# Optimization experiments

Measured on AMD Instinct MI355X. Metric: run time of the kernel, lower is better.

Reference implementation:

```python
import jax, jax.numpy as jnp
import numpy as np

N_NODES = 50000
N_EDGES = 800000
N_GRAPHS = 64
F_IN, HID, EMB = 6, 64, 128


def gcn_conv(x, edge_index, W, b):
    """PyG GCNConv: add self-loops, symmetric deg^{-1/2} normalization, scatter-add."""
    n = x.shape[0]
    loop = jnp.arange(n)
    src = jnp.concatenate([edge_index[0], loop])
    dst = jnp.concatenate([edge_index[1], loop])
    deg = jnp.zeros((n,), x.dtype).at[dst].add(1.0)
    dinv = jnp.where(deg > 0, jax.lax.rsqrt(deg), 0.0)
    norm = dinv[src] * dinv[dst]              # [E+n]
    h = x @ W                                  # [n, out]
    msg = h[src] * norm[:, None]               # gather + scale
    out = jnp.zeros((n, W.shape[1]), h.dtype).at[dst].add(msg)  # scatter-add
    return out + b


def global_mean_pool(x, batch, num_graphs):
    sums = jax.ops.segment_sum(x, batch, num_segments=num_graphs)
    cnts = jax.ops.segment_sum(jnp.ones((x.shape[0],), x.dtype), batch, num_segments=num_graphs)
    return sums / jnp.maximum(cnts, 1.0)[:, None]


def setup_inputs() -> dict:
    key = jax.random.key(0)
    ks = jax.random.split(key, 12)
    x = jax.random.normal(ks[0], (N_NODES, F_IN), dtype=jnp.float32)
    edge_index = jax.random.randint(ks[1], (2, N_EDGES), 0, N_NODES, dtype=jnp.int64 if jax.config.jax_enable_x64 else jnp.int32)
    batch = jnp.sort(jax.random.randint(ks[2], (N_NODES,), 0, N_GRAPHS, dtype=jnp.int32))
    def glorot(k, shp):
        lim = float(np.sqrt(6.0 / (shp[0] + shp[1])))
        return jax.random.uniform(k, shp, jnp.float32, -lim, lim)
    return {
        "x": x, "edge_index": edge_index, "batch": batch,
        "W1": glorot(ks[3], (F_IN, HID)), "b1": jnp.zeros((HID,), jnp.float32),
        "W2": glorot(ks[4], (HID, HID)),  "b2": jnp.zeros((HID,), jnp.float32),
        "W3": glorot(ks[5], (HID, HID)),  "b3": jnp.zeros((HID,), jnp.float32),
        "Wfc": glorot(ks[6], (HID, EMB)), "bfc": jnp.zeros((EMB,), jnp.float32),
    }


def reference(x, edge_index, batch, W1, b1, W2, b2, W3, b3, Wfc, bfc):
    h = jax.nn.relu(gcn_conv(x, edge_index, W1, b1))
    h = jax.nn.relu(gcn_conv(h, edge_index, W2, b2))
    h = jax.nn.relu(gcn_conv(h, edge_index, W3, b3))
    g = global_mean_pool(h, batch, N_GRAPHS)     # [num_graphs, HID]
    return jax.nn.relu(g @ Wfc + bfc)            # [num_graphs, EMB]
```

## Files before the change

kernel.cpp:

```cpp
#include <hip/hip_runtime.h>

#define N_NODES 50000
#define N_EDGES 800000
#define N_GRAPHS 64
#define F_IN 6
#define HID 64
#define EMB 128

#define NBINS 196
#define EPB 4096
#define NCHUNK ((N_EDGES + EPB - 1) / EPB)
#define EPT (EPB / 256)

__global__ void k_init(int* __restrict__ bin_cnt) {
    if (threadIdx.x < NBINS + 4) bin_cnt[threadIdx.x] = 0;
}

__global__ void k_binhist(const int* __restrict__ dst, int* __restrict__ bin_cnt) {
    __shared__ int lcnt[NBINS];
    for (int b = threadIdx.x; b < NBINS; b += 256) lcnt[b] = 0;
    __syncthreads();
    int e0 = blockIdx.x * EPB;
#pragma unroll
    for (int t = 0; t < EPT; ++t) {
        int e = e0 + t * 256 + threadIdx.x;
        if (e < N_EDGES) atomicAdd(&lcnt[dst[e] >> 8], 1);
    }
    __syncthreads();
    for (int b = threadIdx.x; b < NBINS; b += 256) {
        int c = lcnt[b];
        if (c) atomicAdd(&bin_cnt[b], c);
    }
}

__global__ void k_binscan(const int* __restrict__ bin_cnt, int* __restrict__ bin_start,
                          int* __restrict__ bin_pos, int* __restrict__ row_start,
                          float* __restrict__ gsum, float* __restrict__ gcnt) {
    __shared__ int s[256];
    int t = threadIdx.x;
    int v = (t < NBINS) ? bin_cnt[t] : 0;
    s[t] = v;
    __syncthreads();
    for (int off = 1; off < 256; off <<= 1) {
        int o = (t >= off) ? s[t - off] : 0;
        __syncthreads();
        s[t] += o;
        __syncthreads();
    }
    if (t < NBINS) { int st = s[t] - v; bin_start[t] = st; bin_pos[t] = st; }
    if (t == 0) { bin_start[NBINS] = N_EDGES; row_start[N_NODES] = N_EDGES; }
    for (int i = t; i < N_GRAPHS * HID; i += 256) gsum[i] = 0.0f;
    if (t < N_GRAPHS) gcnt[t] = 0.0f;
}

__global__ void k_part(const int* __restrict__ src, const int* __restrict__ dst,
                       int* __restrict__ bin_pos, int* __restrict__ rec) {
    __shared__ int lcnt[NBINS];
    __shared__ int lbase[NBINS];
    for (int b = threadIdx.x; b < NBINS; b += 256) lcnt[b] = 0;
    __syncthreads();
    int e0 = blockIdx.x * EPB;
    int myBin[EPT], myRank[EPT], myRec[EPT];
#pragma unroll
    for (int t = 0; t < EPT; ++t) {
        int e = e0 + t * 256 + threadIdx.x;
        myBin[t] = -1;
        if (e < N_EDGES) {
            int d = dst[e];
            int s = src[e];
            int b = d >> 8;
            myBin[t] = b;
            myRec[t] = (s << 8) | (d & 255);
            myRank[t] = atomicAdd(&lcnt[b], 1);
        }
    }
    __syncthreads();
    for (int b = threadIdx.x; b < NBINS; b += 256) {
        int c = lcnt[b];
        lbase[b] = c ? atomicAdd(&bin_pos[b], c) : 0;
    }
    __syncthreads();
#pragma unroll
    for (int t = 0; t < EPT; ++t)
        if (myBin[t] >= 0) rec[lbase[myBin[t]] + myRank[t]] = myRec[t];
}

__global__ void k_bindeg(const int* __restrict__ rec, const int* __restrict__ bin_start,
                         const float* __restrict__ x, int* __restrict__ row_start,
                         float* __restrict__ dinv, float* __restrict__ xs) {
    __shared__ int ldeg[256];
    __shared__ int s[256];
    int t = threadIdx.x;
    ldeg[t] = 0;
    __syncthreads();
    int beg = bin_start[blockIdx.x], end = bin_start[blockIdx.x + 1];
    for (int r = beg + t; r < end; r += 256)
        atomicAdd(&ldeg[rec[r] & 255], 1);
    __syncthreads();
    int v = ldeg[t];
    s[t] = v;
    __syncthreads();
    for (int off = 1; off < 256; off <<= 1) {
        int o = (t >= off) ? s[t - off] : 0;
        __syncthreads();
        s[t] += o;
        __syncthreads();
    }
    int node = blockIdx.x * 256 + t;
    if (node < N_NODES) {
        row_start[node] = beg + s[t] - v;
        float dv = rsqrtf((float)(v + 1));
        dinv[node] = dv;
#pragma unroll
        for (int k = 0; k < F_IN; ++k) xs[node * F_IN + k] = x[node * F_IN + k] * dv;
    }
}

__global__ void k_fine(const int* __restrict__ rec, const int* __restrict__ bin_start,
                       const int* __restrict__ row_start, int* __restrict__ eidx) {
    __shared__ int lpos[256];
    lpos[threadIdx.x] = 0;
    __syncthreads();
    int beg = bin_start[blockIdx.x], end = bin_start[blockIdx.x + 1];
    int base = blockIdx.x * 256;
    for (int r = beg + threadIdx.x; r < end; r += 256) {
        int rc = rec[r];
        int ld = rc & 255;
        int p = atomicAdd(&lpos[ld], 1);
        eidx[row_start[base + ld] + p] = rc >> 8;
    }
}

__device__ __forceinline__ float bcast(float v, int lane) {
    return __int_as_float(__builtin_amdgcn_readlane(__float_as_int(v), lane));
}

__global__ void k_l1(const float* __restrict__ xs, const int* __restrict__ row_start,
                     const int* __restrict__ eidx, const float* __restrict__ dinv,
                     const float* __restrict__ W1, const float* __restrict__ b1,
                     float* __restrict__ out) {
    __shared__ float sW[F_IN * HID];
    __shared__ float sB[HID];
    for (int i = threadIdx.x; i < F_IN * HID; i += 256) sW[i] = W1[i];
    if (threadIdx.x < HID) sB[threadIdx.x] = b1[threadIdx.x];
    __syncthreads();
    int node = (blockIdx.x * blockDim.x + threadIdx.x) >> 6;
    int f = threadIdx.x & 63;
    if (node >= N_NODES) return;
    int beg = __builtin_amdgcn_readfirstlane(row_start[node]);
    int end = __builtin_amdgcn_readfirstlane(row_start[node + 1]);
    bool act = (f < F_IN);
    float sum = 0.0f;
    int j = beg;
    for (; j + 8 <= end; j += 8) {
        int s0 = eidx[j+0], s1 = eidx[j+1], s2 = eidx[j+2], s3 = eidx[j+3];
        int s4 = eidx[j+4], s5 = eidx[j+5], s6 = eidx[j+6], s7 = eidx[j+7];
        if (act) {
            float v0 = xs[s0 * F_IN + f], v1 = xs[s1 * F_IN + f];
            float v2 = xs[s2 * F_IN + f], v3 = xs[s3 * F_IN + f];
            float v4 = xs[s4 * F_IN + f], v5 = xs[s5 * F_IN + f];
            float v6 = xs[s6 * F_IN + f], v7 = xs[s7 * F_IN + f];
            sum += ((v0 + v1) + (v2 + v3)) + ((v4 + v5) + (v6 + v7));
        }
    }
    for (; j < end; ++j) {
        int s = eidx[j];
        if (act) sum += xs[s * F_IN + f];
    }
    float dv = dinv[node];
    float val = act ? (sum + xs[node * F_IN + f]) * dv : 0.0f;
    float o = sB[f];
    o = fmaf(bcast(val, 0), sW[0 * HID + f], o);
    o = fmaf(bcast(val, 1), sW[1 * HID + f], o);
    o = fmaf(bcast(val, 2), sW[2 * HID + f], o);
    o = fmaf(bcast(val, 3), sW[3 * HID + f], o);
    o = fmaf(bcast(val, 4), sW[4 * HID + f], o);
    o = fmaf(bcast(val, 5), sW[5 * HID + f], o);
    out[node * HID + f] = fmaxf(o, 0.0f);
}

#define MM_BLOCKS 625
__global__ void k_mm(const float* __restrict__ x, const float* __restrict__ W,
                     const float* __restrict__ dinv, float* __restrict__ h) {
    int f = threadIdx.x & 63;
    float wk[HID];
#pragma unroll
    for (int k = 0; k < HID; ++k) wk[k] = W[k * HID + f];
    int wv = blockIdx.x * (blockDim.x >> 6) + (threadIdx.x >> 6);
    const int nwaves = MM_BLOCKS * 4;
    for (int node = wv; node < N_NODES; node += nwaves) {
        float xv = x[node * HID + f];
        float dv = dinv[node];
        float a0 = 0.0f, a1 = 0.0f, a2 = 0.0f, a3 = 0.0f;
#pragma unroll
        for (int k = 0; k < HID; k += 4) {
            a0 = fmaf(bcast(xv, k + 0), wk[k + 0], a0);
            a1 = fmaf(bcast(xv, k + 1), wk[k + 1], a1);
            a2 = fmaf(bcast(xv, k + 2), wk[k + 2], a2);
            a3 = fmaf(bcast(xv, k + 3), wk[k + 3], a3);
        }
        h[node * HID + f] = ((a0 + a1) + (a2 + a3)) * dv;
    }
}

__global__ void k_gather(const float* __restrict__ h, const int* __restrict__ row_start,
                         const int* __restrict__ eidx, const float* __restrict__ dinv,
                         const float* __restrict__ b, float* __restrict__ out) {
    int node = (blockIdx.x * blockDim.x + threadIdx.x) >> 6;
    int f = threadIdx.x & 63;
    if (node >= N_NODES) return;
    int beg = __builtin_amdgcn_readfirstlane(row_start[node]);
    int end = __builtin_amdgcn_readfirstlane(row_start[node + 1]);
    float sum = 0.0f;
    int j = beg;
    for (; j + 8 <= end; j += 8) {
        int s0 = eidx[j+0], s1 = eidx[j+1], s2 = eidx[j+2], s3 = eidx[j+3];
        int s4 = eidx[j+4], s5 = eidx[j+5], s6 = eidx[j+6], s7 = eidx[j+7];
        float v0 = h[s0 * HID + f], v1 = h[s1 * HID + f];
        float v2 = h[s2 * HID + f], v3 = h[s3 * HID + f];
        float v4 = h[s4 * HID + f], v5 = h[s5 * HID + f];
        float v6 = h[s6 * HID + f], v7 = h[s7 * HID + f];
        sum += ((v0 + v1) + (v2 + v3)) + ((v4 + v5) + (v6 + v7));
    }
    if (j + 4 <= end) {
        int s0 = eidx[j+0], s1 = eidx[j+1], s2 = eidx[j+2], s3 = eidx[j+3];
        float v0 = h[s0 * HID + f], v1 = h[s1 * HID + f];
        float v2 = h[s2 * HID + f], v3 = h[s3 * HID + f];
        sum += ((v0 + v1) + (v2 + v3));
        j += 4;
    }
    for (; j < end; ++j) sum += h[eidx[j] * HID + f];
    sum += h[node * HID + f];
    out[node * HID + f] = fmaxf(fmaf(sum, dinv[node], b[f]), 0.0f);
}

#define POOL_BLOCKS 200
__global__ void k_pool(const float* __restrict__ x, const int* __restrict__ batch,
                       float* __restrict__ gsum, float* __restrict__ gcnt) {
    const int npb = (N_NODES + POOL_BLOCKS - 1) / POOL_BLOCKS;
    int start = blockIdx.x * npb;
    int end = start + npb;
    if (end > N_NODES) end = N_NODES;
    int f = threadIdx.x & 63;
    int grp = threadIdx.x >> 6;
    float sum = 0.0f, cnt = 0.0f;
    int curg = -1;
    for (int node = start + grp; node < end; node += 4) {
        int g = batch[node];
        if (g != curg) {
            if (curg >= 0) {
                atomicAdd(&gsum[curg * HID + f], sum);
                if (f == 0) atomicAdd(&gcnt[curg], cnt);
            }
            curg = g; sum = 0.0f; cnt = 0.0f;
        }
        sum += x[node * HID + f];
        cnt += 1.0f;
    }
    if (curg >= 0) {
        atomicAdd(&gsum[curg * HID + f], sum);
        if (f == 0) atomicAdd(&gcnt[curg], cnt);
    }
}

__global__ void k_fc(const float* __restrict__ gsum, const float* __restrict__ gcnt,
                     const float* __restrict__ Wfc, const float* __restrict__ bfc,
                     float* __restrict__ out) {
    int gid = blockIdx.x * blockDim.x + threadIdx.x;
    if (gid >= N_GRAPHS * EMB) return;
    int g = gid >> 7;
    int j = gid & 127;
    float inv = 1.0f / fmaxf(gcnt[g], 1.0f);
    float s = bfc[j];
#pragma unroll 8
    for (int k = 0; k < HID; ++k) s += gsum[g * HID + k] * inv * Wfc[k * EMB + j];
    out[gid] = fmaxf(s, 0.0f);
}

extern "C" void kernel_launch(void* const* d_in, const int* in_sizes, int n_in,
                              void* d_out, int out_size, void* d_ws, size_t ws_size,
                              hipStream_t stream) {
    const float* x    = (const float*)d_in[0];
    const int*   ei   = (const int*)d_in[1];
    const int*   batch= (const int*)d_in[2];
    const float* W1   = (const float*)d_in[3];
    const float* b1   = (const float*)d_in[4];
    const float* W2   = (const float*)d_in[5];
    const float* b2   = (const float*)d_in[6];
    const float* W3   = (const float*)d_in[7];
    const float* b3   = (const float*)d_in[8];
    const float* Wfc  = (const float*)d_in[9];
    const float* bfc  = (const float*)d_in[10];
    float* out = (float*)d_out;

    float* ws        = (float*)d_ws;
    float* dinv      = ws;
    float* h         = ws + 50048;
    float* xcur      = h + N_NODES * HID;
    float* gsum      = xcur + N_NODES * HID;
    float* gcnt      = gsum + N_GRAPHS * HID;
    float* xs        = gcnt + 64;
    int*   row_start = (int*)(xs + 300032);
    int*   bin_cnt   = row_start + 50176;
    int*   bin_start = bin_cnt + 256;
    int*   bin_pos   = bin_start + 256;
    int*   rec       = bin_pos + 256;
    int*   eidx      = rec + 800000;

    const int* src = ei;
    const int* dst = ei + N_EDGES;

    const int B = 256;
    const int gNF = (N_NODES * HID + B - 1) / B;

    k_init<<<1, B, 0, stream>>>(bin_cnt);
    k_binhist<<<NCHUNK, B, 0, stream>>>(dst, bin_cnt);
    k_binscan<<<1, B, 0, stream>>>(bin_cnt, bin_start, bin_pos, row_start, gsum, gcnt);
    k_part<<<NCHUNK, B, 0, stream>>>(src, dst, bin_pos, rec);
    k_bindeg<<<NBINS, B, 0, stream>>>(rec, bin_start, x, row_start, dinv, xs);
    k_fine<<<NBINS, B, 0, stream>>>(rec, bin_start, row_start, eidx);

    k_l1<<<gNF, B, 0, stream>>>(xs, row_start, eidx, dinv, W1, b1, xcur);
    k_mm<<<MM_BLOCKS, B, 0, stream>>>(xcur, W2, dinv, h);
    k_gather<<<gNF, B, 0, stream>>>(h, row_start, eidx, dinv, b2, xcur);
    k_mm<<<MM_BLOCKS, B, 0, stream>>>(xcur, W3, dinv, h);
    k_gather<<<gNF, B, 0, stream>>>(h, row_start, eidx, dinv, b3, xcur);

    k_pool<<<POOL_BLOCKS, B, 0, stream>>>(xcur, batch, gsum, gcnt);
    k_fc<<<(N_GRAPHS * EMB + B - 1) / B, B, 0, stream>>>(gsum, gcnt, Wfc, bfc, out);
}
```

Measured before the change: 206.7 us.

## Fuse neighbor aggregation with following dense transform into persistent kernels

Merges layer-1 aggregation with the W2 matmul, and layer-2 gather with the W3 matmul, into two persistent wave-per-node kernels. The intermediate activations no longer round-trip through global memory, and two launches are removed. In exchange, each wave holds 64 weight registers while gathering, which may lower occupancy and latency hiding in the gather loop, and grid-stride scheduling over 1280 blocks replaces the one-node-per-wave grid.

```diff
diff --git a/kernel.cpp b/kernel.cpp
--- a/kernel.cpp
+++ b/kernel.cpp
@@ -135,71 +135,109 @@
     return __int_as_float(__builtin_amdgcn_readlane(__float_as_int(v), lane));
 }
 
-__global__ void k_l1(const float* __restrict__ xs, const int* __restrict__ row_start,
-                     const int* __restrict__ eidx, const float* __restrict__ dinv,
-                     const float* __restrict__ W1, const float* __restrict__ b1,
-                     float* __restrict__ out) {
+#define PB 1280
+
+__global__ void k_l1mm(const float* __restrict__ xs, const int* __restrict__ row_start,
+                       const int* __restrict__ eidx, const float* __restrict__ dinv,
+                       const float* __restrict__ W1, const float* __restrict__ b1,
+                       const float* __restrict__ W2, float* __restrict__ hout) {
     __shared__ float sW[F_IN * HID];
     __shared__ float sB[HID];
     for (int i = threadIdx.x; i < F_IN * HID; i += 256) sW[i] = W1[i];
     if (threadIdx.x < HID) sB[threadIdx.x] = b1[threadIdx.x];
     __syncthreads();
-    int node = (blockIdx.x * blockDim.x + threadIdx.x) >> 6;
-    int f = threadIdx.x & 63;
-    if (node >= N_NODES) return;
-    int beg = __builtin_amdgcn_readfirstlane(row_start[node]);
-    int end = __builtin_amdgcn_readfirstlane(row_start[node + 1]);
-    bool act = (f < F_IN);
-    float sum = 0.0f;
-    int j = beg;
-    for (; j + 8 <= end; j += 8) {
-        int s0 = eidx[j+0], s1 = eidx[j+1], s2 = eidx[j+2], s3 = eidx[j+3];
-        int s4 = eidx[j+4], s5 = eidx[j+5], s6 = eidx[j+6], s7 = eidx[j+7];
-        if (act) {
-            float v0 = xs[s0 * F_IN + f], v1 = xs[s1 * F_IN + f];
-            float v2 = xs[s2 * F_IN + f], v3 = xs[s3 * F_IN + f];
-            float v4 = xs[s4 * F_IN + f], v5 = xs[s5 * F_IN + f];
-            float v6 = xs[s6 * F_IN + f], v7 = xs[s7 * F_IN + f];
-            sum += ((v0 + v1) + (v2 + v3)) + ((v4 + v5) + (v6 + v7));
-        }
-    }
-    for (; j < end; ++j) {
-        int s = eidx[j];
-        if (act) sum += xs[s * F_IN + f];
-    }
-    float dv = dinv[node];
-    float val = act ? (sum + xs[node * F_IN + f]) * dv : 0.0f;
-    float o = sB[f];
-    o = fmaf(bcast(val, 0), sW[0 * HID + f], o);
-    o = fmaf(bcast(val, 1), sW[1 * HID + f], o);
-    o = fmaf(bcast(val, 2), sW[2 * HID + f], o);
-    o = fmaf(bcast(val, 3), sW[3 * HID + f], o);
-    o = fmaf(bcast(val, 4), sW[4 * HID + f], o);
-    o = fmaf(bcast(val, 5), sW[5 * HID + f], o);
-    out[node * HID + f] = fmaxf(o, 0.0f);
-}
-
-#define MM_BLOCKS 625
-__global__ void k_mm(const float* __restrict__ x, const float* __restrict__ W,
-                     const float* __restrict__ dinv, float* __restrict__ h) {
     int f = threadIdx.x & 63;
     float wk[HID];
 #pragma unroll
-    for (int k = 0; k < HID; ++k) wk[k] = W[k * HID + f];
-    int wv = blockIdx.x * (blockDim.x >> 6) + (threadIdx.x >> 6);
-    const int nwaves = MM_BLOCKS * 4;
-    for (int node = wv; node < N_NODES; node += nwaves) {
-        float xv = x[node * HID + f];
+    for (int k = 0; k < HID; ++k) wk[k] = W2[k * HID + f];
+    bool act = (f < F_IN);
+    int wv = blockIdx.x * 4 + (threadIdx.x >> 6);
+    for (int node = wv; node < N_NODES; node += PB * 4) {
+        int beg = __builtin_amdgcn_readfirstlane(row_start[node]);
+        int end = __builtin_amdgcn_readfirstlane(row_start[node + 1]);
+        float sum = 0.0f;
+        int j = beg;
+        for (; j + 8 <= end; j += 8) {
+            int s0 = eidx[j+0], s1 = eidx[j+1], s2 = eidx[j+2], s3 = eidx[j+3];
+            int s4 = eidx[j+4], s5 = eidx[j+5], s6 = eidx[j+6], s7 = eidx[j+7];
+            if (act) {
+                float v0 = xs[s0 * F_IN + f], v1 = xs[s1 * F_IN + f];
+                float v2 = xs[s2 * F_IN + f], v3 = xs[s3 * F_IN + f];
+                float v4 = xs[s4 * F_IN + f], v5 = xs[s5 * F_IN + f];
+                float v6 = xs[s6 * F_IN + f], v7 = xs[s7 * F_IN + f];
+                sum += ((v0 + v1) + (v2 + v3)) + ((v4 + v5) + (v6 + v7));
+            }
+        }
+        for (; j < end; ++j) {
+            int s = eidx[j];
+            if (act) sum += xs[s * F_IN + f];
+        }
         float dv = dinv[node];
+        float val = act ? (sum + xs[node * F_IN + f]) * dv : 0.0f;
+        float o = sB[f];
+        o = fmaf(bcast(val, 0), sW[0 * HID + f], o);
+        o = fmaf(bcast(val, 1), sW[1 * HID + f], o);
+        o = fmaf(bcast(val, 2), sW[2 * HID + f], o);
+        o = fmaf(bcast(val, 3), sW[3 * HID + f], o);
+        o = fmaf(bcast(val, 4), sW[4 * HID + f], o);
+        o = fmaf(bcast(val, 5), sW[5 * HID + f], o);
+        o = fmaxf(o, 0.0f);
         float a0 = 0.0f, a1 = 0.0f, a2 = 0.0f, a3 = 0.0f;
 #pragma unroll
         for (int k = 0; k < HID; k += 4) {
-            a0 = fmaf(bcast(xv, k + 0), wk[k + 0], a0);
-            a1 = fmaf(bcast(xv, k + 1), wk[k + 1], a1);
-            a2 = fmaf(bcast(xv, k + 2), wk[k + 2], a2);
-            a3 = fmaf(bcast(xv, k + 3), wk[k + 3], a3);
-        }
-        h[node * HID + f] = ((a0 + a1) + (a2 + a3)) * dv;
+            a0 = fmaf(bcast(o, k + 0), wk[k + 0], a0);
+            a1 = fmaf(bcast(o, k + 1), wk[k + 1], a1);
+            a2 = fmaf(bcast(o, k + 2), wk[k + 2], a2);
+            a3 = fmaf(bcast(o, k + 3), wk[k + 3], a3);
+        }
+        hout[node * HID + f] = ((a0 + a1) + (a2 + a3)) * dv;
+    }
+}
+
+__global__ void k_gmm(const float* __restrict__ h, const int* __restrict__ row_start,
+                      const int* __restrict__ eidx, const float* __restrict__ dinv,
+                      const float* __restrict__ b2, const float* __restrict__ W3,
+                      float* __restrict__ hout) {
+    int f = threadIdx.x & 63;
+    float wk[HID];
+#pragma unroll
+    for (int k = 0; k < HID; ++k) wk[k] = W3[k * HID + f];
+    float bv = b2[f];
+    int wv = blockIdx.x * 4 + (threadIdx.x >> 6);
+    for (int node = wv; node < N_NODES; node += PB * 4) {
+        int beg = __builtin_amdgcn_readfirstlane(row_start[node]);
+        int end = __builtin_amdgcn_readfirstlane(row_start[node + 1]);
+        float sum = 0.0f;
+        int j = beg;
+        for (; j + 8 <= end; j += 8) {
+            int s0 = eidx[j+0], s1 = eidx[j+1], s2 = eidx[j+2], s3 = eidx[j+3];
+            int s4 = eidx[j+4], s5 = eidx[j+5], s6 = eidx[j+6], s7 = eidx[j+7];
+            float v0 = h[s0 * HID + f], v1 = h[s1 * HID + f];
+            float v2 = h[s2 * HID + f], v3 = h[s3 * HID + f];
+            float v4 = h[s4 * HID + f], v5 = h[s5 * HID + f];
+            float v6 = h[s6 * HID + f], v7 = h[s7 * HID + f];
+            sum += ((v0 + v1) + (v2 + v3)) + ((v4 + v5) + (v6 + v7));
+        }
+        if (j + 4 <= end) {
+            int s0 = eidx[j+0], s1 = eidx[j+1], s2 = eidx[j+2], s3 = eidx[j+3];
+            float v0 = h[s0 * HID + f], v1 = h[s1 * HID + f];
+            float v2 = h[s2 * HID + f], v3 = h[s3 * HID + f];
+            sum += ((v0 + v1) + (v2 + v3));
+            j += 4;
+        }
+        for (; j < end; ++j) sum += h[eidx[j] * HID + f];
+        sum += h[node * HID + f];
+        float dv = dinv[node];
+        float o = fmaxf(fmaf(sum, dv, bv), 0.0f);
+        float a0 = 0.0f, a1 = 0.0f, a2 = 0.0f, a3 = 0.0f;
+#pragma unroll
+        for (int k = 0; k < HID; k += 4) {
+            a0 = fmaf(bcast(o, k + 0), wk[k + 0], a0);
+            a1 = fmaf(bcast(o, k + 1), wk[k + 1], a1);
+            a2 = fmaf(bcast(o, k + 2), wk[k + 2], a2);
+            a3 = fmaf(bcast(o, k + 3), wk[k + 3], a3);
+        }
+        hout[node * HID + f] = ((a0 + a1) + (a2 + a3)) * dv;
     }
 }
 
@@ -320,12 +358,10 @@
     k_bindeg<<<NBINS, B, 0, stream>>>(rec, bin_start, x, row_start, dinv, xs);
     k_fine<<<NBINS, B, 0, stream>>>(rec, bin_start, row_start, eidx);
 
-    k_l1<<<gNF, B, 0, stream>>>(xs, row_start, eidx, dinv, W1, b1, xcur);
-    k_mm<<<MM_BLOCKS, B, 0, stream>>>(xcur, W2, dinv, h);
-    k_gather<<<gNF, B, 0, stream>>>(h, row_start, eidx, dinv, b2, xcur);
-    k_mm<<<MM_BLOCKS, B, 0, stream>>>(xcur, W3, dinv, h);
-    k_gather<<<gNF, B, 0, stream>>>(h, row_start, eidx, dinv, b3, xcur);
-
-    k_pool<<<POOL_BLOCKS, B, 0, stream>>>(xcur, batch, gsum, gcnt);
+    k_l1mm<<<PB, B, 0, stream>>>(xs, row_start, eidx, dinv, W1, b1, W2, h);
+    k_gmm<<<PB, B, 0, stream>>>(h, row_start, eidx, dinv, b2, W3, xcur);
+    k_gather<<<gNF, B, 0, stream>>>(xcur, row_start, eidx, dinv, b3, h);
+
+    k_pool<<<POOL_BLOCKS, B, 0, stream>>>(h, batch, gsum, gcnt);
     k_fc<<<(N_GRAPHS * EMB + B - 1) / B, B, 0, stream>>>(gsum, gcnt, Wfc, bfc, out);
 }
```

After: 178.8 us. 13.5% less time.
